# Kernel optimization log

Measured on AMD Instinct MI355X. Metric: run time of the kernel, lower is better.

## Reference

```python
import math
import jax, jax.numpy as jnp
import numpy as np

NUM_HEAD = 16

def get_slopes(n):
    def pow2(n):
        start = 2 ** (-2 ** (-(math.log2(n) - 3)))
        return [start * start ** i for i in range(n)]
    if math.log2(n).is_integer():
        return pow2(n)
    c = 2 ** math.floor(math.log2(n))
    return pow2(c) + get_slopes(2 * c)[0::2][: n - c]

def setup_inputs() -> dict:
    key = jax.random.key(0)
    ks = jax.random.split(key, 9)
    B, T, C = 2, 2048, 2048
    x = jax.random.normal(ks[0], (B, T, C), dtype=jnp.float32)
    std = 0.02
    Wq = std * jax.random.normal(ks[1], (C, C), dtype=jnp.float32)
    Wk = std * jax.random.normal(ks[2], (C, C), dtype=jnp.float32)
    Wv = std * jax.random.normal(ks[3], (C, C), dtype=jnp.float32)
    Wo = (0.02 / np.sqrt(2 * 24)) * jax.random.normal(ks[4], (C, C), dtype=jnp.float32)
    bq = jnp.zeros((C,), jnp.float32)
    bk = jnp.zeros((C,), jnp.float32)
    bv = jnp.zeros((C,), jnp.float32)
    bo = jnp.zeros((C,), jnp.float32)
    return {"x": x, "Wq": Wq, "bq": bq, "Wk": Wk, "bk": bk,
            "Wv": Wv, "bv": bv, "Wo": Wo, "bo": bo}

def reference(x, Wq, bq, Wk, bk, Wv, bv, Wo, bo):
    B, T, C = x.shape
    H = NUM_HEAD
    D = C // H
    slopes = jnp.asarray(get_slopes(H), dtype=jnp.float32)  # [H]

    def split_heads(y):  # [B,T,C] -> [B,H,T,D]
        return y.reshape(B, T, H, D).transpose(0, 2, 1, 3)

    q = split_heads(x @ Wq + bq)
    k = split_heads(x @ Wk + bk)
    v = split_heads(x @ Wv + bv)

    attn = jnp.einsum("bhqd,bhkd->bhqk", q, k) / jnp.sqrt(jnp.float32(D))
    # ALiBi: bias[h, j] = slopes[h] * (j - (T-1)), broadcast over queries
    alibi = slopes[:, None, None] * (jnp.arange(T, dtype=jnp.float32) - (T - 1))[None, None, :]
    attn = attn + alibi  # [B,H,T,T] + [H,1,T]

    causal = jnp.tril(jnp.ones((T, T), dtype=bool))[None, None]
    attn = jnp.where(causal, attn, jnp.finfo(jnp.float32).min)
    p = jax.nn.softmax(attn, axis=-1)

    o = jnp.einsum("bhqk,bhkd->bhqd", p, v).transpose(0, 2, 1, 3).reshape(B, T, C)
    return o @ Wo + bo
```

## Files before the change

kernel.cpp:

```cpp
#include <hip/hip_runtime.h>
#include <math.h>


typedef unsigned short u16;
using bf16x8 = __attribute__((ext_vector_type(8))) short;
using f32x4  = __attribute__((ext_vector_type(4))) float;

__device__ __forceinline__ u16 f2bf(float f) {
  union { float f; unsigned u; } c; c.f = f;
  unsigned r = c.u + 0x7fffu + ((c.u >> 16) & 1u);
  return (u16)(r >> 16);
}
__device__ __forceinline__ float bf2f(u16 b) {
  union { unsigned u; float f; } c; c.u = ((unsigned)b) << 16; return c.f;
}
__device__ __forceinline__ unsigned cvtpk(float a, float b) {
  unsigned r;
  asm("v_cvt_pk_bf16_f32 %0, %1, %2" : "=v"(r) : "v"(a), "v"(b));
  return r;
}
__device__ __forceinline__ void g2l16(const void* g, void* l) {
  __builtin_amdgcn_global_load_lds(
      (const __attribute__((address_space(1))) void*)g,
      (__attribute__((address_space(3))) void*)l, 16, 0, 0);
}

__device__ __forceinline__ int band_jmin(int s, float slope2) {
  const int idist = (int)(36.0f / slope2);
  const int cut = 64 * s - idist - 31;
  return (cut > 0) ? (cut >> 5) : 0;
}

__global__ __launch_bounds__(256) void split_f32(const float* __restrict__ in,
                                                 u16* __restrict__ hi, int n4) {
  for (int i = blockIdx.x * 256 + threadIdx.x; i < n4; i += gridDim.x * 256) {
    const float4 v = ((const float4*)in)[i];
    ushort4 h;
    h.x = f2bf(v.x); h.y = f2bf(v.y); h.z = f2bf(v.z); h.w = f2bf(v.w);
    ((ushort4*)hi)[i] = h;
  }
}

__global__ __launch_bounds__(256) void tsplit4_f32(
    const float* __restrict__ W0, const float* __restrict__ W1,
    const float* __restrict__ W2, const float* __restrict__ W3,
    u16* __restrict__ D0, u16* __restrict__ D1,
    u16* __restrict__ D2, u16* __restrict__ D3,
    int N, int K, float sc0) {
  __shared__ float tile[64][68];
  const int z = blockIdx.z;
  const float* W = (z == 0) ? W0 : (z == 1) ? W1 : (z == 2) ? W2 : W3;
  u16* Wth = (z == 0) ? D0 : (z == 1) ? D1 : (z == 2) ? D2 : D3;
  const float sc = (z == 0) ? sc0 : 1.f;
  const int tid = threadIdx.x;
  const int k0 = blockIdx.y * 64, n0 = blockIdx.x * 64;
  const int rr = tid >> 4, cc = (tid & 15) * 4;
#pragma unroll
  for (int u = 0; u < 4; ++u) {
    const float4 v = *(const float4*)&W[(size_t)(k0 + rr + 16 * u) * N + n0 + cc];
    tile[rr + 16 * u][cc + 0] = v.x;
    tile[rr + 16 * u][cc + 1] = v.y;
    tile[rr + 16 * u][cc + 2] = v.z;
    tile[rr + 16 * u][cc + 3] = v.w;
  }
  __syncthreads();
#pragma unroll
  for (int u = 0; u < 4; ++u) {
    const int nn = rr + 16 * u;
    ushort4 h;
    h.x = f2bf(tile[cc + 0][nn] * sc);
    h.y = f2bf(tile[cc + 1][nn] * sc);
    h.z = f2bf(tile[cc + 2][nn] * sc);
    h.w = f2bf(tile[cc + 3][nn] * sc);
    *(ushort4*)&Wth[(size_t)(n0 + nn) * K + k0 + cc] = h;
  }
}

template <int MODE>
__global__ __launch_bounds__(512, 4) void gemm256x128(
    const u16* __restrict__ Ah, const u16* __restrict__ Bth,
    const float* __restrict__ bias, const float* __restrict__ bias2,
    float bsc, u16* __restrict__ outH, u16* __restrict__ outH2,
    float* __restrict__ outF, int MM, int NN, int KK) {
  __shared__ u16 LA[3][8192];
  __shared__ u16 LB[3][4096];

  const int tid = threadIdx.x;
  const int wave = tid >> 6, lane = tid & 63;
  const int g = lane >> 4, q15 = lane & 15;
  const int wr = wave >> 1, wc = wave & 1;
  const int m0 = blockIdx.y * 256, n0 = blockIdx.x * 128;
  const int NT = KK >> 5;
  const int sxg = ((g ^ ((q15 >> 1) & 3)) << 4);

  f32x4 acc[4][4];
#pragma unroll
  for (int f = 0; f < 4; ++f)
#pragma unroll
    for (int j = 0; j < 4; ++j) acc[f][j] = (f32x4){0.f, 0.f, 0.f, 0.f};

  auto stageA = [&](int t, int rbuf) {
#pragma unroll
    for (int l = 0; l < 2; ++l) {
      const int ch = l * 512 + tid;
      const int row = ch >> 2, slot = ch & 3;
      const size_t ga = (size_t)(m0 + row) * KK + t * 32 +
                        ((slot ^ ((row >> 1) & 3)) * 8);
      g2l16(Ah + ga, (char*)(LA[rbuf]) + ch * 16);
    }
  };
  auto stageB = [&](int t, int rbuf) {
    const int ch = tid;
    const int row = ch >> 2, slot = ch & 3;
    const size_t gb = (size_t)(n0 + row) * KK + t * 32 +
                      ((slot ^ ((row >> 1) & 3)) * 8);
    g2l16(Bth + gb, (char*)(LB[rbuf]) + ch * 16);
  };

  stageA(0, 0); stageB(0, 0);
  __builtin_amdgcn_sched_barrier(0);
  if (NT > 1) { stageA(1, 1); stageB(1, 1); }
  __builtin_amdgcn_sched_barrier(0);
  if (NT > 1) { asm volatile("s_waitcnt vmcnt(3)" ::: "memory"); }
  else        { asm volatile("s_waitcnt vmcnt(0)" ::: "memory"); }
  __builtin_amdgcn_sched_barrier(0);
  __builtin_amdgcn_s_barrier();

  int rb = 0, rb2 = 2;
  for (int t = 0; t < NT; ++t) {
    const char* baseA = (const char*)(LA[rb]);
    const char* baseB = (const char*)(LB[rb]);

    bf16x8 af[4], bf[4];
#pragma unroll
    for (int f = 0; f < 4; ++f)
      af[f] = *(const bf16x8*)(baseA + (wr * 64 + f * 16 + q15) * 64 + sxg);
#pragma unroll
    for (int j = 0; j < 4; ++j)
      bf[j] = *(const bf16x8*)(baseB + (wc * 64 + j * 16 + q15) * 64 + sxg);
    if (t + 2 < NT) { stageA(t + 2, rb2); stageB(t + 2, rb2); }
    __builtin_amdgcn_sched_barrier(0);
    __builtin_amdgcn_s_barrier();
    asm volatile("s_waitcnt lgkmcnt(0)" ::: "memory");
    __builtin_amdgcn_sched_barrier(0);
    __builtin_amdgcn_s_setprio(1);
#pragma unroll
    for (int f = 0; f < 4; ++f)
#pragma unroll
      for (int j = 0; j < 4; ++j)
        acc[f][j] = __builtin_amdgcn_mfma_f32_16x16x32_bf16(
            af[f], bf[j], acc[f][j], 0, 0, 0);
    __builtin_amdgcn_s_setprio(0);
    if (t + 1 < NT) {
      if (t + 2 < NT) { asm volatile("s_waitcnt vmcnt(3)" ::: "memory"); }
      else            { asm volatile("s_waitcnt vmcnt(0)" ::: "memory"); }
    }
    __builtin_amdgcn_sched_barrier(0);
    __builtin_amdgcn_s_barrier();
    rb  = (rb  == 2) ? 0 : rb  + 1;
    rb2 = (rb2 == 2) ? 0 : rb2 + 1;
  }

#pragma unroll
  for (int f = 0; f < 4; ++f)
#pragma unroll
    for (int j = 0; j < 4; ++j)
#pragma unroll
      for (int r = 0; r < 4; ++r) {
        const int row = m0 + wr * 64 + f * 16 + g * 4 + r;
        const int col = n0 + wc * 64 + j * 16 + q15;
        const float v = acc[f][j][r];
        if (MODE == 0) {
          outF[(size_t)row * NN + col] = v + bias[col] * bsc;
        } else if (MODE == 2) {
          outH[(size_t)row * NN + col] = f2bf(v + bias[row] * bsc);
        } else {
          const int sel = col >> 11;
          const int c2 = col & 2047;
          const float vv = v + (sel ? bias2[c2] : bias[c2] * bsc);
          const int bb = row >> 11, tt = row & 2047;
          const int hh = c2 >> 7, dd = c2 & 127;
          (sel ? outH2 : outH)[(((size_t)bb * 16 + hh) * 2048 + tt) * 128 + dd] =
              f2bf(vv);
        }
      }
}

__global__ __launch_bounds__(64) void attn_splitk(
    const u16* __restrict__ Qh, const u16* __restrict__ Kh,
    const u16* __restrict__ Vth, u16* __restrict__ Oh,
    float* __restrict__ Obuf, float* __restrict__ mArr,
    float* __restrict__ lArr, int T, int NB, int BH) {
  __shared__ u16 KS[3][4096];

  const int tid = threadIdx.x;
  const int lane = tid & 63;
  const int g = lane >> 4, q15 = lane & 15;
  const int L = blockIdx.x;
  const int LL = L >> 1;
  const int wid = L & 1;

  int bh, u;
  if (BH == 32) {
    const int k = LL >> 8;
    const int c = LL & 255;
    bh = (c + 5 * k) & 31;
    u = k * 8 + (c >> 5);
  } else {
    bh = LL / 48;
    u = LL % 48;
  }
  int s, half;
  if (u < 16)      { s = u;      half = 2; }
  else if (u < 32) { s = 47 - u; half = 0; }
  else             { s = 63 - u; half = 1; }

  const int b = bh >> 4, h = bh & 15;
  const float slope2 = exp2f(-0.5f * (float)(h + 1)) * 1.44269504f;
  const int jmin = band_jmin(s, slope2);
  const bool loEmpty = (jmin >= s + 1);

  if (half == 0 && loEmpty) return;

  int lo, hi;
  if (half == 2)      { lo = jmin;                hi = 2 * s + 2; }
  else if (half == 0) { lo = jmin;                hi = s + 1; }
  else                { lo = loEmpty ? jmin : (s + 1); hi = 2 * s + 2; }
  const int ns = hi - lo;
  const bool maskable = (half != 0);
  const bool normStore = (half == 2) || (half == 1 && loEmpty);

  const int qw0 = s * 64 + wid * 32;
  const size_t vrow0 = (size_t)h * 128;
  const size_t vcol0 = (size_t)b * T;
  const size_t kbase = (size_t)bh * T;

  bf16x8 qfr[2][4];
#pragma unroll
  for (int qf2 = 0; qf2 < 2; ++qf2) {
    const size_t rb = ((size_t)bh * T + qw0 + qf2 * 16 + q15) * 128;
#pragma unroll
    for (int ks = 0; ks < 4; ++ks)
      qfr[qf2][ks] = *(const bf16x8*)&Qh[rb + ks * 32 + g * 8];
  }

  f32x4 oacc[2][8];
#pragma unroll
  for (int a = 0; a < 2; ++a)
#pragma unroll
    for (int n = 0; n < 8; ++n) oacc[a][n] = (f32x4){0.f, 0.f, 0.f, 0.f};
  float m_st[2] = {-1e5f, -1e5f};
  float l_part[2] = {0.f, 0.f};

  auto stageK = [&](int jt, int bf) {
    const int j0 = jt * 32;
#pragma unroll
    for (int c = 0; c < 8; ++c) {
      const int row = c * 4 + g;
      const int off = (q15 * 16) ^ ((row & 7) << 4);
      const size_t gb = (kbase + j0 + row) * 128;
      g2l16((const char*)(Kh + gb) + off, (char*)(KS[bf]) + c * 1024);
    }
  };
  auto loadV = [&](int jt, bf16x8 (&vf)[8]) {
    const int j0 = jt * 32;
#pragma unroll
    for (int nf = 0; nf < 8; ++nf)
      vf[nf] = *(const bf16x8*)
          &Vth[(vrow0 + nf * 16 + q15) * (size_t)NB + vcol0 + j0 + g * 8];
  };

  bf16x8 vfA[8], vfB[8];
  __builtin_amdgcn_sched_barrier(0);
  stageK(hi - 1, 0);
  if (ns > 1) stageK(hi - 2, 1);
  __builtin_amdgcn_sched_barrier(0);
  loadV(hi - 1, vfA);
  if (ns > 1) { asm volatile("s_waitcnt vmcnt(16)" ::: "memory"); }
  else        { asm volatile("s_waitcnt vmcnt(8)"  ::: "memory"); }
  __builtin_amdgcn_sched_barrier(0);

  int cur = 0;

  auto ITER = [&](int it, bf16x8 (&vc)[8], bf16x8 (&vn)[8]) {
    const int jt = hi - 1 - it;
    const int j0 = jt * 32;

    const bool haveV1 = (it + 1 < ns);
    const bool haveK2 = (it + 2 < ns);
    if (haveV1) loadV(jt - 1, vn);
    if (haveK2) {
      int nb = cur + 2; if (nb >= 3) nb -= 3;
      stageK(jt - 2, nb);
    }
    __builtin_amdgcn_sched_barrier(0);

    f32x4 sacc[2][2];
#pragma unroll
    for (int jf = 0; jf < 2; ++jf)
#pragma unroll
      for (int qf2 = 0; qf2 < 2; ++qf2) sacc[jf][qf2] = (f32x4){0.f, 0.f, 0.f, 0.f};
#pragma unroll
    for (int ks = 0; ks < 4; ++ks) {
      bf16x8 ka[2];
#pragma unroll
      for (int jf = 0; jf < 2; ++jf) {
        const int row = jf * 16 + q15;
        const int off = (row * 256 + ks * 64 + g * 16) ^ ((row & 7) << 4);
        ka[jf] = *(const bf16x8*)((const char*)(KS[cur]) + off);
      }
#pragma unroll
      for (int jf = 0; jf < 2; ++jf)
#pragma unroll
        for (int qf2 = 0; qf2 < 2; ++qf2)
          sacc[jf][qf2] = __builtin_amdgcn_mfma_f32_16x16x32_bf16(
              ka[jf], qfr[qf2][ks], sacc[jf][qf2], 0, 0, 0);
    }

    const float jb2 = (float)(j0 + 4 * g - (T - 1));

    unsigned Fw[2][4];
#pragma unroll
    for (int qf2 = 0; qf2 < 2; ++qf2) {
      const int qg = qw0 + qf2 * 16 + q15;
      float sv[2][4];
      float mt = -1e30f;
#pragma unroll
      for (int jf = 0; jf < 2; ++jf)
#pragma unroll
        for (int r = 0; r < 4; ++r) {
          float x = fmaf(slope2, jb2 + (float)(jf * 16 + r), sacc[jf][qf2][r]);
          if (maskable && it < 2) {
            const int jg = j0 + jf * 16 + 4 * g + r;
            x = (jg > qg) ? -1e30f : x;
          }
          sv[jf][r] = x;
          mt = fmaxf(mt, x);
        }
      if (!__all(mt <= m_st[qf2] + 11.0f)) {
        mt = fmaxf(mt, __shfl_xor(mt, 16));
        mt = fmaxf(mt, __shfl_xor(mt, 32));
        const float mnew = fmaxf(m_st[qf2], mt);
        const float scl = exp2f(m_st[qf2] - mnew);
        l_part[qf2] *= scl;
        m_st[qf2] = mnew;
#pragma unroll
        for (int r = 0; r < 4; ++r) {
          const float sc = __shfl(scl, g * 4 + r);
#pragma unroll
          for (int nf = 0; nf < 8; ++nf) oacc[qf2][nf][r] *= sc;
        }
      }
      float rs = 0.f;
      float p[2][4];
#pragma unroll
      for (int jf = 0; jf < 2; ++jf)
#pragma unroll
        for (int r = 0; r < 4; ++r) {
          p[jf][r] = exp2f(sv[jf][r] - m_st[qf2]);
          rs += p[jf][r];
        }
      l_part[qf2] += rs;
      const unsigned W00 = cvtpk(p[0][0], p[0][1]), W01 = cvtpk(p[0][2], p[0][3]);
      const unsigned W10 = cvtpk(p[1][0], p[1][1]), W11 = cvtpk(p[1][2], p[1][3]);
      const int srcA = q15 + ((g & 1) << 5);
      const int srcB = srcA + 16;
      const unsigned A0 = (unsigned)__shfl((int)W00, srcA);
      const unsigned A1 = (unsigned)__shfl((int)W01, srcA);
      const unsigned B0 = (unsigned)__shfl((int)W00, srcB);
      const unsigned B1 = (unsigned)__shfl((int)W01, srcB);
      const unsigned C0 = (unsigned)__shfl((int)W10, srcA);
      const unsigned C1 = (unsigned)__shfl((int)W11, srcA);
      const unsigned D0 = (unsigned)__shfl((int)W10, srcB);
      const unsigned D1 = (unsigned)__shfl((int)W11, srcB);
      const bool hi2 = g >= 2;
      Fw[qf2][0] = hi2 ? C0 : A0;
      Fw[qf2][1] = hi2 ? C1 : A1;
      Fw[qf2][2] = hi2 ? D0 : B0;
      Fw[qf2][3] = hi2 ? D1 : B1;
    }

    if (haveV1) {
      if (haveK2) { asm volatile("s_waitcnt vmcnt(16)" ::: "memory"); }
      else        { asm volatile("s_waitcnt vmcnt(8)"  ::: "memory"); }
    } else        { asm volatile("s_waitcnt vmcnt(0)"  ::: "memory"); }
    __builtin_amdgcn_sched_barrier(0);

    union { unsigned uu[4]; bf16x8 v; } pa0, pa1;
#pragma unroll
    for (int w = 0; w < 4; ++w) { pa0.uu[w] = Fw[0][w]; pa1.uu[w] = Fw[1][w]; }
#pragma unroll
    for (int nf = 0; nf < 8; ++nf) {
      oacc[0][nf] = __builtin_amdgcn_mfma_f32_16x16x32_bf16(pa0.v, vc[nf], oacc[0][nf], 0, 0, 0);
      oacc[1][nf] = __builtin_amdgcn_mfma_f32_16x16x32_bf16(pa1.v, vc[nf], oacc[1][nf], 0, 0, 0);
    }

    cur = (cur == 2) ? 0 : cur + 1;
  };

  for (int it = 0; it < ns;) {
    ITER(it, vfA, vfB); ++it;
    if (it >= ns) break;
    ITER(it, vfB, vfA); ++it;
  }

  float lrow[2];
#pragma unroll
  for (int qf2 = 0; qf2 < 2; ++qf2) {
    float lr = l_part[qf2];
    lr += __shfl_xor(lr, 16);
    lr += __shfl_xor(lr, 32);
    lrow[qf2] = lr;
  }

  if (normStore) {
#pragma unroll
    for (int qf2 = 0; qf2 < 2; ++qf2) {
      const float inv = 1.0f / lrow[qf2];
#pragma unroll
      for (int r = 0; r < 4; ++r) {
        const float iv = __shfl(inv, g * 4 + r);
        const int qrow = qw0 + qf2 * 16 + g * 4 + r;
        const size_t ob = ((size_t)b * T + qrow) * 2048 + h * 128;
#pragma unroll
        for (int nf = 0; nf < 8; ++nf)
          Oh[ob + nf * 16 + q15] = f2bf(oacc[qf2][nf][r] * iv);
      }
    }
  } else {
    const int sp = s - 16;
    const size_t sbase = ((size_t)(bh * 16 + sp) * 2 + half) * 64;
    if (g == 0) {
#pragma unroll
      for (int qf2 = 0; qf2 < 2; ++qf2) {
        mArr[sbase + wid * 32 + qf2 * 16 + q15] = m_st[qf2];
        lArr[sbase + wid * 32 + qf2 * 16 + q15] = lrow[qf2];
      }
    }
    const size_t obase = sbase * 128;
#pragma unroll
    for (int qf2 = 0; qf2 < 2; ++qf2)
#pragma unroll
      for (int r = 0; r < 4; ++r) {
        const int row = wid * 32 + qf2 * 16 + g * 4 + r;
#pragma unroll
        for (int nf = 0; nf < 8; ++nf)
          Obuf[obase + (size_t)row * 128 + nf * 16 + q15] = oacc[qf2][nf][r];
      }
  }
}

__global__ __launch_bounds__(128) void combine_halves(
    const float* __restrict__ Obuf, const float* __restrict__ mArr,
    const float* __restrict__ lArr, u16* __restrict__ Oh, int T) {
  const int idx = blockIdx.x;
  const int row = idx & 63;
  const int sp = (idx >> 6) & 15;
  const int bh = idx >> 10;
  const int d = threadIdx.x;
  const int s = sp + 16;
  const int b = bh >> 4, h = bh & 15;
  const float slope2 = exp2f(-0.5f * (float)(h + 1)) * 1.44269504f;
  if (band_jmin(s, slope2) >= s + 1) return;
  const size_t sbase = ((size_t)(bh * 16 + sp) * 2) * 64;
  const float m1 = mArr[sbase + row],      l1 = lArr[sbase + row];
  const float m2 = mArr[sbase + 64 + row], l2 = lArr[sbase + 64 + row];
  const float M = fmaxf(m1, m2);
  const float w1 = exp2f(m1 - M), w2 = exp2f(m2 - M);
  const float inv = 1.0f / (l1 * w1 + l2 * w2);
  const size_t ob = sbase * 128;
  const float o1 = Obuf[ob + (size_t)row * 128 + d];
  const float o2 = Obuf[ob + 8192 + (size_t)row * 128 + d];
  const float v = (o1 * w1 + o2 * w2) * inv;
  const int qrow = s * 64 + row;
  Oh[((size_t)b * T + qrow) * 2048 + h * 128 + d] = f2bf(v);
}

#define TM 128
#define BKG 8

template <int QKV>
__global__ __launch_bounds__(256) void gemm_f32(
    const float* __restrict__ A, const float* __restrict__ W,
    const float* __restrict__ bias, float* __restrict__ out,
    int M, int N, int K, int T) {
  __shared__ float As[BKG][TM];
  __shared__ float Bs[BKG][TM];
  const int tid = threadIdx.x;
  const int tx = tid & 15, ty = tid >> 4;
  const int m0 = blockIdx.y * TM, n0 = blockIdx.x * TM;
  float acc[8][8];
#pragma unroll
  for (int i = 0; i < 8; ++i)
#pragma unroll
    for (int j = 0; j < 8; ++j) acc[i][j] = 0.f;
  const int arow = tid >> 1, acol = (tid & 1) * 4;
  const int brow = tid >> 5, bcol = (tid & 31) * 4;
  for (int k0 = 0; k0 < K; k0 += BKG) {
    const float4 av = *(const float4*)&A[(size_t)(m0 + arow) * K + k0 + acol];
    const float4 bv = *(const float4*)&W[(size_t)(k0 + brow) * N + n0 + bcol];
    __syncthreads();
    As[acol + 0][arow] = av.x; As[acol + 1][arow] = av.y;
    As[acol + 2][arow] = av.z; As[acol + 3][arow] = av.w;
    *(float4*)&Bs[brow][bcol] = bv;
    __syncthreads();
#pragma unroll
    for (int kk = 0; kk < BKG; ++kk) {
      const float4 a0 = *(const float4*)&As[kk][ty * 4];
      const float4 a1 = *(const float4*)&As[kk][64 + ty * 4];
      const float4 b0 = *(const float4*)&Bs[kk][tx * 4];
      const float4 b1 = *(const float4*)&Bs[kk][64 + tx * 4];
      const float af[8] = {a0.x, a0.y, a0.z, a0.w, a1.x, a1.y, a1.z, a1.w};
      const float bf[8] = {b0.x, b0.y, b0.z, b0.w, b1.x, b1.y, b1.z, b1.w};
#pragma unroll
      for (int i = 0; i < 8; ++i)
#pragma unroll
        for (int j = 0; j < 8; ++j) acc[i][j] += af[i] * bf[j];
    }
  }
#pragma unroll
  for (int a = 0; a < 2; ++a)
#pragma unroll
    for (int i = 0; i < 4; ++i) {
      const int row = m0 + a * 64 + ty * 4 + i;
      const int bb = row / T, t = row % T;
#pragma unroll
      for (int bj = 0; bj < 2; ++bj) {
        const int col = n0 + bj * 64 + tx * 4;
        float4 r;
        r.x = acc[a * 4 + i][bj * 4 + 0] + bias[col + 0];
        r.y = acc[a * 4 + i][bj * 4 + 1] + bias[col + 1];
        r.z = acc[a * 4 + i][bj * 4 + 2] + bias[col + 2];
        r.w = acc[a * 4 + i][bj * 4 + 3] + bias[col + 3];
        if (QKV) {
          const int hh = col >> 7, dd = col & 127;
          *(float4*)&out[(((size_t)bb * 16 + hh) * T + t) * 128 + dd] = r;
        } else {
          *(float4*)&out[(size_t)row * N + col] = r;
        }
      }
    }
}

#define QT 32
#define KT 32
#define DP 132

__global__ __launch_bounds__(256) void flash_f32(
    const float* __restrict__ Q, const float* __restrict__ K,
    const float* __restrict__ V, float* __restrict__ O, int T) {
  __shared__ float Qs[QT][DP];
  __shared__ float Ks[KT][DP];
  __shared__ float Vs[KT][DP];
  __shared__ float Ps[QT][KT + 1];
  const int tid = threadIdx.x;
  const int jh = tid & 15, ih = tid >> 4;
  const int bh = blockIdx.y;
  const int h = bh & 15;
  const int q0 = blockIdx.x * QT;
  const float slope = exp2f(-0.5f * (float)(h + 1));
  const float rsD = 0.08838834764831845f;
  {
    const float* Qg = Q + ((size_t)bh * T + q0) * 128;
    const int r = tid >> 3, p = tid & 7;
#pragma unroll
    for (int u = 0; u < 4; ++u)
      *(float4*)&Qs[r][(p + 8 * u) * 4] = *(const float4*)&Qg[r * 128 + (p + 8 * u) * 4];
  }
  float m_st[2] = {-1e30f, -1e30f};
  float l_st[2] = {0.f, 0.f};
  float accv[2][8] = {};
  const int ktiles = blockIdx.x + 1;
  for (int kt = 0; kt < ktiles; ++kt) {
    const int j0 = kt * KT;
    const float* Kg = K + ((size_t)bh * T + j0) * 128;
    const float* Vg = V + ((size_t)bh * T + j0) * 128;
    __syncthreads();
    {
      const int r = tid >> 3, p = tid & 7;
#pragma unroll
      for (int u = 0; u < 4; ++u) {
        *(float4*)&Ks[r][(p + 8 * u) * 4] = *(const float4*)&Kg[r * 128 + (p + 8 * u) * 4];
        *(float4*)&Vs[r][(p + 8 * u) * 4] = *(const float4*)&Vg[r * 128 + (p + 8 * u) * 4];
      }
    }
    __syncthreads();
    float s00 = 0.f, s01 = 0.f, s10 = 0.f, s11 = 0.f;
#pragma unroll 8
    for (int d4 = 0; d4 < 32; ++d4) {
      const float4 qa = *(const float4*)&Qs[2 * ih + 0][4 * d4];
      const float4 qb = *(const float4*)&Qs[2 * ih + 1][4 * d4];
      const float4 ka = *(const float4*)&Ks[2 * jh + 0][4 * d4];
      const float4 kb = *(const float4*)&Ks[2 * jh + 1][4 * d4];
      s00 += qa.x * ka.x + qa.y * ka.y + qa.z * ka.z + qa.w * ka.w;
      s01 += qa.x * kb.x + qa.y * kb.y + qa.z * kb.z + qa.w * kb.w;
      s10 += qb.x * ka.x + qb.y * ka.y + qb.z * ka.z + qb.w * ka.w;
      s11 += qb.x * kb.x + qb.y * kb.y + qb.z * kb.z + qb.w * kb.w;
    }
    float sc[2][2] = {{s00, s01}, {s10, s11}};
    float mt[2];
#pragma unroll
    for (int r = 0; r < 2; ++r) {
      const int qg = q0 + 2 * ih + r;
#pragma unroll
      for (int c = 0; c < 2; ++c) {
        const int jg = j0 + 2 * jh + c;
        const float svv = sc[r][c] * rsD + slope * (float)(jg - (T - 1));
        sc[r][c] = (jg > qg) ? -1e30f : svv;
      }
      mt[r] = fmaxf(sc[r][0], sc[r][1]);
    }
#pragma unroll
    for (int m = 1; m < 16; m <<= 1) {
      mt[0] = fmaxf(mt[0], __shfl_xor(mt[0], m));
      mt[1] = fmaxf(mt[1], __shfl_xor(mt[1], m));
    }
#pragma unroll
    for (int r = 0; r < 2; ++r) {
      const float mnew = fmaxf(m_st[r], mt[r]);
      const float scl = (m_st[r] > -1e29f) ? expf(m_st[r] - mnew) : 0.f;
      const float p0 = expf(sc[r][0] - mnew);
      const float p1 = expf(sc[r][1] - mnew);
      float rs = p0 + p1;
#pragma unroll
      for (int m = 1; m < 16; m <<= 1) rs += __shfl_xor(rs, m);
      l_st[r] = l_st[r] * scl + rs;
      m_st[r] = mnew;
#pragma unroll
      for (int d = 0; d < 8; ++d) accv[r][d] *= scl;
      Ps[2 * ih + r][2 * jh + 0] = p0;
      Ps[2 * ih + r][2 * jh + 1] = p1;
    }
    __syncthreads();
#pragma unroll 4
    for (int j = 0; j < KT; ++j) {
      const float p0 = Ps[2 * ih + 0][j];
      const float p1 = Ps[2 * ih + 1][j];
      const float4 v0 = *(const float4*)&Vs[j][8 * jh];
      const float4 v1 = *(const float4*)&Vs[j][8 * jh + 4];
      accv[0][0] += p0 * v0.x; accv[0][1] += p0 * v0.y;
      accv[0][2] += p0 * v0.z; accv[0][3] += p0 * v0.w;
      accv[0][4] += p0 * v1.x; accv[0][5] += p0 * v1.y;
      accv[0][6] += p0 * v1.z; accv[0][7] += p0 * v1.w;
      accv[1][0] += p1 * v0.x; accv[1][1] += p1 * v0.y;
      accv[1][2] += p1 * v0.z; accv[1][3] += p1 * v0.w;
      accv[1][4] += p1 * v1.x; accv[1][5] += p1 * v1.y;
      accv[1][6] += p1 * v1.z; accv[1][7] += p1 * v1.w;
    }
  }
  const int b = bh >> 4;
#pragma unroll
  for (int r = 0; r < 2; ++r) {
    const int qg = q0 + 2 * ih + r;
    const float inv = 1.0f / l_st[r];
    float4 o0, o1;
    o0.x = accv[r][0] * inv; o0.y = accv[r][1] * inv;
    o0.z = accv[r][2] * inv; o0.w = accv[r][3] * inv;
    o1.x = accv[r][4] * inv; o1.y = accv[r][5] * inv;
    o1.z = accv[r][6] * inv; o1.w = accv[r][7] * inv;
    float* dst = O + ((size_t)b * T + qg) * 2048 + h * 128 + 8 * jh;
    *(float4*)&dst[0] = o0;
    *(float4*)&dst[4] = o1;
  }
}

extern "C" void kernel_launch(void* const* d_in, const int* in_sizes, int n_in,
                              void* d_out, int out_size, void* d_ws,
                              size_t ws_size, hipStream_t stream) {
  const float* x  = (const float*)d_in[0];
  const float* Wq = (const float*)d_in[1];
  const float* bq = (const float*)d_in[2];
  const float* Wk = (const float*)d_in[3];
  const float* bk = (const float*)d_in[4];
  const float* Wv = (const float*)d_in[5];
  const float* bv = (const float*)d_in[6];
  const float* Wo = (const float*)d_in[7];
  const float* bo = (const float*)d_in[8];
  float* out = (float*)d_out;

  const int C = 2048, T = 2048, H = 16;
  const int M = in_sizes[0] / C;
  const int B = M / T;
  const int BH = B * H;
  const size_t MC = (size_t)M * C, CC = (size_t)C * C;
  const size_t splitO = (size_t)BH * 16 * 2 * 8192;
  const size_t splitML = (size_t)BH * 16 * 2 * 64;
  const size_t need = (5 * MC + 4 * CC) * sizeof(u16) +
                      (splitO + 2 * splitML) * sizeof(float);

  const float QSC = 0.08838834764831845f * 1.44269504088896f;

  if (ws_size >= need && (M % 256) == 0) {
    u16* p = (u16*)d_ws;
    u16* xh   = p; p += MC;
    u16* wqth = p; p += CC;
    u16* wkth = p; p += CC;
    u16* wvth = p; p += CC;
    u16* woth = p; p += CC;
    u16* qh   = p; p += MC;
    u16* kh   = p; p += MC;
    u16* vth  = p; p += MC;
    u16* oh   = p; p += MC;
    float* Obuf = (float*)p;
    float* mArr = Obuf + splitO;
    float* lArr = mArr + splitML;

    split_f32<<<1024, 256, 0, stream>>>(x, xh, (int)(MC / 4));
    dim3 tg(C / 64, C / 64, 4);
    tsplit4_f32<<<tg, 256, 0, stream>>>(Wq, Wk, Wv, Wo, wqth, wkth, wvth,
                                        woth, C, C, QSC);

    dim3 gqk(2 * C / 128, M / 256);
    gemm256x128<3><<<gqk, 512, 0, stream>>>(xh, wqth, bq, bk, QSC, qh, kh,
                                            nullptr, M, 2 * C, C);
    dim3 gv(M / 128, C / 256);
    gemm256x128<2><<<gv, 512, 0, stream>>>(wvth, xh, bv, nullptr, 1.f, vth,
                                           nullptr, nullptr, C, M, C);

    attn_splitk<<<96 * BH, 64, 0, stream>>>(qh, kh, vth, oh, Obuf, mArr,
                                            lArr, T, M, BH);
    combine_halves<<<BH * 16 * 64, 128, 0, stream>>>(Obuf, mArr, lArr, oh, T);

    dim3 gq(C / 128, M / 256);
    gemm256x128<0><<<gq, 512, 0, stream>>>(oh, woth, bo, nullptr, 1.f,
                                           nullptr, nullptr, out, M, C, C);
  } else {
    float* Qw = (float*)d_ws;
    float* Kw = Qw + MC;
    float* Vw = Kw + MC;
    float* Ow = Vw + MC;
    dim3 ggrid(C / TM, M / TM);
    gemm_f32<1><<<ggrid, 256, 0, stream>>>(x, Wq, bq, Qw, M, C, C, T);
    gemm_f32<1><<<ggrid, 256, 0, stream>>>(x, Wk, bk, Kw, M, C, C, T);
    gemm_f32<1><<<ggrid, 256, 0, stream>>>(x, Wv, bv, Vw, M, C, C, T);
    dim3 fgrid(T / QT, B * H);
    flash_f32<<<fgrid, 256, 0, stream>>>(Qw, Kw, Vw, Ow, T);
    gemm_f32<0><<<ggrid, 256, 0, stream>>>(Ow, Wo, bo, out, M, C, C, T);
  }
}
```

Measured before the change: 291.8 us.

## Shrink GEMM tiles to 128x128 with double buffering, reorder attention work, raise MFMA priority

The projection GEMMs move from a 256x128 tile with 512 threads and a triple-buffered LDS pipeline to a 128x128 tile with 256 threads and a simpler double-buffered pipeline. That doubles the block count and cuts LDS per block, at the cost of less reuse per tile and a full vmcnt(0) wait every k-step. Attention blocks are remapped through a lookup table so the longest band segments are scheduled first, to improve load balance. setprio is also raised around the MFMA sections in attention.

```diff
diff --git a/kernel.cpp b/kernel.cpp
--- a/kernel.cpp
+++ b/kernel.cpp
@@ -30,6 +30,13 @@
   const int cut = 64 * s - idist - 31;
   return (cut > 0) ? (cut >> 5) : 0;
 }
+
+__device__ const unsigned char uord[48] = {
+  15, 16, 32, 17, 33, 14, 18, 34, 19, 35,
+  13, 20, 36, 21, 37, 12, 22, 38, 23, 39,
+  11, 24, 40, 25, 41, 10, 26, 42, 27, 43,
+   9, 28, 44, 29, 45,  8, 30, 46, 31, 47,
+   7,  6,  5,  4,  3,  2,  1,  0};
 
 __global__ __launch_bounds__(256) void split_f32(const float* __restrict__ in,
                                                  u16* __restrict__ hi, int n4) {
@@ -77,19 +84,19 @@
 }
 
 template <int MODE>
-__global__ __launch_bounds__(512, 4) void gemm256x128(
+__global__ __launch_bounds__(256) void gemm128(
     const u16* __restrict__ Ah, const u16* __restrict__ Bth,
     const float* __restrict__ bias, const float* __restrict__ bias2,
     float bsc, u16* __restrict__ outH, u16* __restrict__ outH2,
     float* __restrict__ outF, int MM, int NN, int KK) {
-  __shared__ u16 LA[3][8192];
-  __shared__ u16 LB[3][4096];
+  __shared__ u16 LA[2][4096];
+  __shared__ u16 LB[2][4096];
 
   const int tid = threadIdx.x;
   const int wave = tid >> 6, lane = tid & 63;
   const int g = lane >> 4, q15 = lane & 15;
   const int wr = wave >> 1, wc = wave & 1;
-  const int m0 = blockIdx.y * 256, n0 = blockIdx.x * 128;
+  const int m0 = blockIdx.y * 128, n0 = blockIdx.x * 128;
   const int NT = KK >> 5;
   const int sxg = ((g ^ ((q15 >> 1) & 3)) << 4);
 
@@ -102,7 +109,7 @@
   auto stageA = [&](int t, int rbuf) {
 #pragma unroll
     for (int l = 0; l < 2; ++l) {
-      const int ch = l * 512 + tid;
+      const int ch = l * 256 + tid;
       const int row = ch >> 2, slot = ch & 3;
       const size_t ga = (size_t)(m0 + row) * KK + t * 32 +
                         ((slot ^ ((row >> 1) & 3)) * 8);
@@ -110,26 +117,25 @@
     }
   };
   auto stageB = [&](int t, int rbuf) {
-    const int ch = tid;
-    const int row = ch >> 2, slot = ch & 3;
-    const size_t gb = (size_t)(n0 + row) * KK + t * 32 +
-                      ((slot ^ ((row >> 1) & 3)) * 8);
-    g2l16(Bth + gb, (char*)(LB[rbuf]) + ch * 16);
+#pragma unroll
+    for (int l = 0; l < 2; ++l) {
+      const int ch = l * 256 + tid;
+      const int row = ch >> 2, slot = ch & 3;
+      const size_t gb = (size_t)(n0 + row) * KK + t * 32 +
+                        ((slot ^ ((row >> 1) & 3)) * 8);
+      g2l16(Bth + gb, (char*)(LB[rbuf]) + ch * 16);
+    }
   };
 
   stageA(0, 0); stageB(0, 0);
-  __builtin_amdgcn_sched_barrier(0);
-  if (NT > 1) { stageA(1, 1); stageB(1, 1); }
-  __builtin_amdgcn_sched_barrier(0);
-  if (NT > 1) { asm volatile("s_waitcnt vmcnt(3)" ::: "memory"); }
-  else        { asm volatile("s_waitcnt vmcnt(0)" ::: "memory"); }
+  asm volatile("s_waitcnt vmcnt(0)" ::: "memory");
   __builtin_amdgcn_sched_barrier(0);
   __builtin_amdgcn_s_barrier();
 
-  int rb = 0, rb2 = 2;
   for (int t = 0; t < NT; ++t) {
-    const char* baseA = (const char*)(LA[rb]);
-    const char* baseB = (const char*)(LB[rb]);
+    const int d = t & 1;
+    const char* baseA = (const char*)(LA[d]);
+    const char* baseB = (const char*)(LB[d]);
 
     bf16x8 af[4], bf[4];
 #pragma unroll
@@ -138,10 +144,7 @@
 #pragma unroll
     for (int j = 0; j < 4; ++j)
       bf[j] = *(const bf16x8*)(baseB + (wc * 64 + j * 16 + q15) * 64 + sxg);
-    if (t + 2 < NT) { stageA(t + 2, rb2); stageB(t + 2, rb2); }
-    __builtin_amdgcn_sched_barrier(0);
-    __builtin_amdgcn_s_barrier();
-    asm volatile("s_waitcnt lgkmcnt(0)" ::: "memory");
+    if (t + 1 < NT) { stageA(t + 1, d ^ 1); stageB(t + 1, d ^ 1); }
     __builtin_amdgcn_sched_barrier(0);
     __builtin_amdgcn_s_setprio(1);
 #pragma unroll
@@ -152,13 +155,10 @@
             af[f], bf[j], acc[f][j], 0, 0, 0);
     __builtin_amdgcn_s_setprio(0);
     if (t + 1 < NT) {
-      if (t + 2 < NT) { asm volatile("s_waitcnt vmcnt(3)" ::: "memory"); }
-      else            { asm volatile("s_waitcnt vmcnt(0)" ::: "memory"); }
-    }
-    __builtin_amdgcn_sched_barrier(0);
-    __builtin_amdgcn_s_barrier();
-    rb  = (rb  == 2) ? 0 : rb  + 1;
-    rb2 = (rb2 == 2) ? 0 : rb2 + 1;
+      asm volatile("s_waitcnt vmcnt(0)" ::: "memory");
+      __builtin_amdgcn_sched_barrier(0);
+      __builtin_amdgcn_s_barrier();
+    }
   }
 
 #pragma unroll
@@ -205,10 +205,10 @@
     const int k = LL >> 8;
     const int c = LL & 255;
     bh = (c + 5 * k) & 31;
-    u = k * 8 + (c >> 5);
+    u = uord[k * 8 + (c >> 5)];
   } else {
     bh = LL / 48;
-    u = LL % 48;
+    u = uord[LL % 48];
   }
   int s, half;
   if (u < 16)      { s = u;      half = 2; }
@@ -300,6 +300,7 @@
     for (int jf = 0; jf < 2; ++jf)
 #pragma unroll
       for (int qf2 = 0; qf2 < 2; ++qf2) sacc[jf][qf2] = (f32x4){0.f, 0.f, 0.f, 0.f};
+    __builtin_amdgcn_s_setprio(1);
 #pragma unroll
     for (int ks = 0; ks < 4; ++ks) {
       bf16x8 ka[2];
@@ -316,6 +317,7 @@
           sacc[jf][qf2] = __builtin_amdgcn_mfma_f32_16x16x32_bf16(
               ka[jf], qfr[qf2][ks], sacc[jf][qf2], 0, 0, 0);
     }
+    __builtin_amdgcn_s_setprio(0);
 
     const float jb2 = (float)(j0 + 4 * g - (T - 1));
 
@@ -389,11 +391,13 @@
     union { unsigned uu[4]; bf16x8 v; } pa0, pa1;
 #pragma unroll
     for (int w = 0; w < 4; ++w) { pa0.uu[w] = Fw[0][w]; pa1.uu[w] = Fw[1][w]; }
+    __builtin_amdgcn_s_setprio(1);
 #pragma unroll
     for (int nf = 0; nf < 8; ++nf) {
       oacc[0][nf] = __builtin_amdgcn_mfma_f32_16x16x32_bf16(pa0.v, vc[nf], oacc[0][nf], 0, 0, 0);
       oacc[1][nf] = __builtin_amdgcn_mfma_f32_16x16x32_bf16(pa1.v, vc[nf], oacc[1][nf], 0, 0, 0);
     }
+    __builtin_amdgcn_s_setprio(0);
 
     cur = (cur == 2) ? 0 : cur + 1;
   };
@@ -710,20 +714,20 @@
     tsplit4_f32<<<tg, 256, 0, stream>>>(Wq, Wk, Wv, Wo, wqth, wkth, wvth,
                                         woth, C, C, QSC);
 
-    dim3 gqk(2 * C / 128, M / 256);
-    gemm256x128<3><<<gqk, 512, 0, stream>>>(xh, wqth, bq, bk, QSC, qh, kh,
-                                            nullptr, M, 2 * C, C);
-    dim3 gv(M / 128, C / 256);
-    gemm256x128<2><<<gv, 512, 0, stream>>>(wvth, xh, bv, nullptr, 1.f, vth,
-                                           nullptr, nullptr, C, M, C);
+    dim3 gqk(2 * C / 128, M / 128);
+    gemm128<3><<<gqk, 256, 0, stream>>>(xh, wqth, bq, bk, QSC, qh, kh,
+                                        nullptr, M, 2 * C, C);
+    dim3 gv(M / 128, C / 128);
+    gemm128<2><<<gv, 256, 0, stream>>>(wvth, xh, bv, nullptr, 1.f, vth,
+                                       nullptr, nullptr, C, M, C);
 
     attn_splitk<<<96 * BH, 64, 0, stream>>>(qh, kh, vth, oh, Obuf, mArr,
                                             lArr, T, M, BH);
     combine_halves<<<BH * 16 * 64, 128, 0, stream>>>(Obuf, mArr, lArr, oh, T);
 
-    dim3 gq(C / 128, M / 256);
-    gemm256x128<0><<<gq, 512, 0, stream>>>(oh, woth, bo, nullptr, 1.f,
-                                           nullptr, nullptr, out, M, C, C);
+    dim3 gq(C / 128, M / 128);
+    gemm128<0><<<gq, 256, 0, stream>>>(oh, woth, bo, nullptr, 1.f,
+                                       nullptr, nullptr, out, M, C, C);
   } else {
     float* Qw = (float*)d_ws;
     float* Kw = Qw + MC;
```

Result: slower. 302.5 us (+3.6%).
